# Kernel tuning notes

Measured on AMD Instinct MI355X. Metric: run time of the kernel, lower is better.

The kernel has to match this reference:

```python
import jax, jax.numpy as jnp
import numpy as np

T, B, I, H, O = 512, 128, 512, 1024, 256

def setup_inputs() -> dict:
    key = jax.random.key(0)
    ks = jax.random.split(key, 7)
    s = 1.0 / np.sqrt(H)
    return {
        "seqs": jax.random.normal(ks[0], (T, B, I), dtype=jnp.float32),
        "W_ih": jax.random.uniform(ks[1], (H, I), minval=-s, maxval=s, dtype=jnp.float32),
        "W_hh": jax.random.uniform(ks[2], (H, H), minval=-s, maxval=s, dtype=jnp.float32),
        "b_ih": jax.random.uniform(ks[3], (H,), minval=-s, maxval=s, dtype=jnp.float32),
        "b_hh": jax.random.uniform(ks[4], (H,), minval=-s, maxval=s, dtype=jnp.float32),
        "W_fc": jax.random.uniform(ks[5], (O, H), minval=-s, maxval=s, dtype=jnp.float32),
        "b_fc": jax.random.uniform(ks[6], (O,), minval=-s, maxval=s, dtype=jnp.float32),
    }

def reference(seqs, W_ih, W_hh, b_ih, b_hh, W_fc, b_fc):
    # Precompute input projections for all timesteps in one big GEMM: [T,B,H]
    x_proj = jnp.einsum('tbi,hi->tbh', seqs, W_ih) + b_ih + b_hh

    def step(h, xp):
        h_new = jax.nn.relu(xp + h @ W_hh.T)
        return h_new, None

    h0 = jnp.zeros((seqs.shape[1], W_hh.shape[0]), dtype=seqs.dtype)
    h_final, _ = jax.lax.scan(step, h0, x_proj)
    return h_final @ W_fc.T + b_fc
```

## Files before the change

kernel.cpp:

```cpp
#include <hip/hip_runtime.h>
#include <hip/hip_bf16.h>
#include <stdint.h>

#define T_STEPS 512
#define BATCH   128
#define IN      512
#define HID     1024
#define OUTN    256

typedef __bf16 bf16x8 __attribute__((ext_vector_type(8)));
typedef float  f32x4  __attribute__((ext_vector_type(4)));
typedef unsigned short us8 __attribute__((ext_vector_type(8)));
typedef unsigned int   ui4 __attribute__((ext_vector_type(4)));

__device__ __forceinline__ unsigned short f2bf(float f) {
    uint32_t u = __float_as_uint(f);
    uint32_t r = (u + 0x7fffu + ((u >> 16) & 1u)) >> 16;
    return (unsigned short)r;
}

__device__ __forceinline__ ui4 ld_u128_agent(const void* p) {
    ui4 v;
    asm volatile("global_load_dwordx4 %0, %1, off sc0 sc1"
                 : "=v"(v) : "v"(p) : "memory");
    return v;
}

__device__ __forceinline__ bf16x8 ld_frag(const unsigned short* smem, int row, int kbyte, int rowstride) {
    int off = row * rowstride + (kbyte ^ ((row & 7) << 4));
    return *reinterpret_cast<const bf16x8*>(reinterpret_cast<const char*>(smem) + off);
}

__global__ __launch_bounds__(256, 1) void rnn_persistent(
    const float* __restrict__ seqs, const float* __restrict__ W_ih,
    const float* __restrict__ W_hh, const float* __restrict__ b_ih,
    const float* __restrict__ b_hh, const float* __restrict__ W_fc,
    const float* __restrict__ b_fc, float* __restrict__ out,
    unsigned short* __restrict__ hbuf,
    float* __restrict__ hfinal,
    unsigned int* __restrict__ flags)
{
    const int tid  = threadIdx.x;
    const int lane = tid & 63;
    const int wv   = tid >> 6;
    const int wg   = blockIdx.x;
    const int g    = wg >> 5;
    const int w    = wg & 31;
    const int gr0  = g * 16;
    const int c0   = w * 32;
    const int ln15 = lane & 15;
    const int lk   = lane >> 4;

    __shared__ unsigned short xtile[16 * 512];
    __shared__ float red[4][16][33];
    __shared__ float biasS[32];

    bf16x8 wih[2][4];
    bf16x8 whh[2][8];
    #pragma unroll
    for (int nt = 0; nt < 2; nt++) {
        const int j = c0 + nt * 16 + ln15;
        #pragma unroll
        for (int s = 0; s < 4; s++) {
            const int k = wv * 128 + s * 32 + lk * 8;
            const float* p = W_ih + j * IN + k;
            us8 u;
            #pragma unroll
            for (int e = 0; e < 8; e++) u[e] = f2bf(p[e]);
            wih[nt][s] = __builtin_bit_cast(bf16x8, u);
        }
        #pragma unroll
        for (int s = 0; s < 8; s++) {
            const int k = wv * 256 + s * 32 + lk * 8;
            const float* p = W_hh + j * HID + k;
            us8 u;
            #pragma unroll
            for (int e = 0; e < 8; e++) u[e] = f2bf(p[e]);
            whh[nt][s] = __builtin_bit_cast(bf16x8, u);
        }
    }
    if (tid < 32) biasS[tid] = b_ih[c0 + tid] + b_hh[c0 + tid];

    unsigned int* grp_flags = flags + g * 32 * 16;
    unsigned int* my_flag   = grp_flags + w * 16;

    const int hfrag = ln15 * 2048 + wv * 512 + lk * 16;

    const int xrow[4] = { (tid) >> 6, (tid + 256) >> 6, (tid + 512) >> 6, (tid + 768) >> 6 };
    const int xcol[4] = { (tid) & 63, (tid + 256) & 63, (tid + 512) & 63, (tid + 768) & 63 };

    us8 xbf[4];
    {
        const float* xsrc = seqs + (size_t)gr0 * IN;
        #pragma unroll
        for (int it = 0; it < 4; it++) {
            const float* s4 = xsrc + xrow[it] * IN + xcol[it] * 8;
            float4 a = *reinterpret_cast<const float4*>(s4);
            float4 b = *reinterpret_cast<const float4*>(s4 + 4);
            us8 u;
            u[0]=f2bf(a.x); u[1]=f2bf(a.y); u[2]=f2bf(a.z); u[3]=f2bf(a.w);
            u[4]=f2bf(b.x); u[5]=f2bf(b.y); u[6]=f2bf(b.z); u[7]=f2bf(b.w);
            xbf[it] = u;
        }
    }

    const size_t slotB = (size_t)BATCH * HID * 2;
    char* hbase = reinterpret_cast<char*>(hbuf);

    for (int t = 0; t < T_STEPS; t++) {
        #pragma unroll
        for (int it = 0; it < 4; it++) {
            const int off = xrow[it] * 1024 + ((xcol[it] * 16) ^ ((xrow[it] & 7) << 4));
            *reinterpret_cast<us8*>(reinterpret_cast<char*>(xtile) + off) = xbf[it];
        }

        float4 xr[8];
        {
            const int tn = (t + 1 < T_STEPS) ? t + 1 : t;
            const float* xsrc = seqs + (size_t)tn * (BATCH * IN) + (size_t)gr0 * IN;
            #pragma unroll
            for (int it = 0; it < 4; it++) {
                const float* s4 = xsrc + xrow[it] * IN + xcol[it] * 8;
                xr[2*it]   = *reinterpret_cast<const float4*>(s4);
                xr[2*it+1] = *reinterpret_cast<const float4*>(s4 + 4);
            }
        }

        if (t > 0 && wv == 0 && lane < 32) {
            const unsigned int* f = grp_flags + lane * 16;
            while (__hip_atomic_load(f, __ATOMIC_RELAXED, __HIP_MEMORY_SCOPE_AGENT) < (unsigned)t) {
                __builtin_amdgcn_s_sleep(1);
            }
        }
        __syncthreads();

        ui4 hv[8];
        if (t > 0) {
            const char* hsrc = hbase + (size_t)(t & 1) * slotB + (size_t)gr0 * 2048 + hfrag;
            #pragma unroll
            for (int s = 0; s < 8; s++) hv[s] = ld_u128_agent(hsrc + s * 64);
        }
        __builtin_amdgcn_sched_barrier(0);

        f32x4 acc0 = {0.f, 0.f, 0.f, 0.f};
        f32x4 acc1 = {0.f, 0.f, 0.f, 0.f};
        {
            const int kx0b = wv * 256;
            #pragma unroll
            for (int s = 0; s < 4; s++) {
                bf16x8 a = ld_frag(xtile, ln15, kx0b + s * 64 + lk * 16, 1024);
                acc0 = __builtin_amdgcn_mfma_f32_16x16x32_bf16(a, wih[0][s], acc0, 0, 0, 0);
                acc1 = __builtin_amdgcn_mfma_f32_16x16x32_bf16(a, wih[1][s], acc1, 0, 0, 0);
            }
        }

        if (t > 0) {
            asm volatile("s_waitcnt vmcnt(0)" ::: "memory");
            __builtin_amdgcn_sched_barrier(0);
            #pragma unroll
            for (int s = 0; s < 8; s++) {
                bf16x8 a = __builtin_bit_cast(bf16x8, hv[s]);
                acc0 = __builtin_amdgcn_mfma_f32_16x16x32_bf16(a, whh[0][s], acc0, 0, 0, 0);
                acc1 = __builtin_amdgcn_mfma_f32_16x16x32_bf16(a, whh[1][s], acc1, 0, 0, 0);
            }
        }

        #pragma unroll
        for (int r = 0; r < 4; r++) {
            red[wv][lk * 4 + r][ln15]      = acc0[r];
            red[wv][lk * 4 + r][16 + ln15] = acc1[r];
        }
        __syncthreads();

        const int hrow = tid >> 4;
        const int co2  = (tid & 15) * 2;
        float v0 = red[0][hrow][co2]   + red[1][hrow][co2]   + red[2][hrow][co2]   + red[3][hrow][co2]   + biasS[co2];
        float v1 = red[0][hrow][co2+1] + red[1][hrow][co2+1] + red[2][hrow][co2+1] + red[3][hrow][co2+1] + biasS[co2+1];
        v0 = fmaxf(v0, 0.0f);
        v1 = fmaxf(v1, 0.0f);

        if (t < T_STEPS - 1) {
            unsigned pack = (unsigned)f2bf(v0) | ((unsigned)f2bf(v1) << 16);
            unsigned* dst = reinterpret_cast<unsigned*>(
                hbase + (size_t)((t + 1) & 1) * slotB
                + ((size_t)(gr0 + hrow) * HID + c0 + co2) * 2);
            __hip_atomic_store(dst, pack, __ATOMIC_RELAXED, __HIP_MEMORY_SCOPE_AGENT);
        } else {
            unsigned long long pack = ((unsigned long long)__float_as_uint(v1) << 32) | __float_as_uint(v0);
            unsigned long long* dst = reinterpret_cast<unsigned long long*>(
                hfinal + (size_t)(gr0 + hrow) * HID + c0 + co2);
            __hip_atomic_store(dst, pack, __ATOMIC_RELAXED, __HIP_MEMORY_SCOPE_AGENT);
        }

        asm volatile("s_waitcnt vmcnt(0)" ::: "memory");
        __builtin_amdgcn_sched_barrier(0);
        __syncthreads();
        if (tid == 0) {
            __hip_atomic_store(my_flag, (unsigned)(t + 1), __ATOMIC_RELAXED, __HIP_MEMORY_SCOPE_AGENT);
        }

        #pragma unroll
        for (int it = 0; it < 4; it++) {
            float4 a = xr[2*it], b = xr[2*it+1];
            us8 u;
            u[0]=f2bf(a.x); u[1]=f2bf(a.y); u[2]=f2bf(a.z); u[3]=f2bf(a.w);
            u[4]=f2bf(b.x); u[5]=f2bf(b.y); u[6]=f2bf(b.z); u[7]=f2bf(b.w);
            xbf[it] = u;
        }
    }

    if (wv == 0 && lane < 32) {
        const unsigned int* f = grp_flags + lane * 16;
        while (__hip_atomic_load(f, __ATOMIC_RELAXED, __HIP_MEMORY_SCOPE_AGENT) < (unsigned)T_STEPS) {
            __builtin_amdgcn_s_sleep(1);
        }
    }
    __syncthreads();
    __threadfence();

    {
        const int oi   = tid & 127;
        const int half = tid >> 7;
        const int brow = gr0 + (oi >> 3);
        const int o    = w * 8 + (oi & 7);
        const float* hv2 = hfinal + (size_t)brow * HID + half * 512;
        const float* wf  = W_fc  + (size_t)o * HID + half * 512;
        float sum = 0.f;
        #pragma unroll 4
        for (int k = 0; k < 512; k += 4) {
            float4 hh = *reinterpret_cast<const float4*>(hv2 + k);
            float4 ww = *reinterpret_cast<const float4*>(wf + k);
            sum += hh.x * ww.x + hh.y * ww.y + hh.z * ww.z + hh.w * ww.w;
        }
        float* redf = &red[0][0][0];
        redf[tid] = sum;
        __syncthreads();
        if (tid < 128) {
            out[(size_t)brow * OUTN + o] = redf[tid] + redf[tid + 128] + b_fc[o];
        }
    }
}

extern "C" void kernel_launch(void* const* d_in, const int* in_sizes, int n_in,
                              void* d_out, int out_size, void* d_ws, size_t ws_size,
                              hipStream_t stream) {
    const float* seqs = (const float*)d_in[0];
    const float* W_ih = (const float*)d_in[1];
    const float* W_hh = (const float*)d_in[2];
    const float* b_ih = (const float*)d_in[3];
    const float* b_hh = (const float*)d_in[4];
    const float* W_fc = (const float*)d_in[5];
    const float* b_fc = (const float*)d_in[6];
    float* out = (float*)d_out;

    char* ws = (char*)d_ws;
    unsigned short* hbuf   = (unsigned short*)ws;
    float*          hfinal = (float*)(ws + 524288);
    unsigned int*   flags  = (unsigned int*)(ws + 1048576);

    hipMemsetAsync(flags, 0, 8 * 32 * 64, stream);
    rnn_persistent<<<dim3(256), dim3(256), 0, stream>>>(
        seqs, W_ih, W_hh, b_ih, b_hh, W_fc, b_fc, out, hbuf, hfinal, flags);
}
```

Before: 1.543 ms.

## Add dedicated poller wavefront with per-producer LDS ready flags and streamed h loads

Adds a fifth wavefront that polls the 32 producer flags and publishes per-producer readiness into LDS. Compute wavefronts can then start loading and multiplying each h chunk as soon as its producer finishes, instead of waiting for the whole group behind a block barrier. The h buffer is re-laid out in producer-contiguous 1KB chunks, and the x tile prefetch is moved two steps ahead. The cost is an extra busy-spinning wave, LDS spin loops without sleep, and more complex synchronisation.

```diff
diff --git a/kernel.cpp b/kernel.cpp
--- a/kernel.cpp
+++ b/kernel.cpp
@@ -22,7 +22,13 @@
 __device__ __forceinline__ ui4 ld_u128_agent(const void* p) {
     ui4 v;
     asm volatile("global_load_dwordx4 %0, %1, off sc0 sc1"
-                 : "=v"(v) : "v"(p) : "memory");
+                 : "=&v"(v) : "v"(p) : "memory");
+    return v;
+}
+__device__ __forceinline__ float4 ld_f128(const void* p) {
+    float4 v;
+    asm volatile("global_load_dwordx4 %0, %1, off"
+                 : "=&v"(v) : "v"(p) : "memory");
     return v;
 }
 
@@ -31,7 +37,11 @@
     return *reinterpret_cast<const bf16x8*>(reinterpret_cast<const char*>(smem) + off);
 }
 
-__global__ __launch_bounds__(256, 1) void rnn_persistent(
+__device__ __forceinline__ void lds_wait(const unsigned* p, unsigned t) {
+    while (__hip_atomic_load(p, __ATOMIC_RELAXED, __HIP_MEMORY_SCOPE_WORKGROUP) < t) { }
+}
+
+__global__ __launch_bounds__(320, 1) void rnn_persistent(
     const float* __restrict__ seqs, const float* __restrict__ W_ih,
     const float* __restrict__ W_hh, const float* __restrict__ b_ih,
     const float* __restrict__ b_hh, const float* __restrict__ W_fc,
@@ -54,43 +64,48 @@
     __shared__ unsigned short xtile[16 * 512];
     __shared__ float red[4][16][33];
     __shared__ float biasS[32];
+    __shared__ unsigned ready[32];
 
     bf16x8 wih[2][4];
     bf16x8 whh[2][8];
-    #pragma unroll
-    for (int nt = 0; nt < 2; nt++) {
-        const int j = c0 + nt * 16 + ln15;
+    if (wv < 4) {
         #pragma unroll
-        for (int s = 0; s < 4; s++) {
-            const int k = wv * 128 + s * 32 + lk * 8;
-            const float* p = W_ih + j * IN + k;
-            us8 u;
-            #pragma unroll
-            for (int e = 0; e < 8; e++) u[e] = f2bf(p[e]);
-            wih[nt][s] = __builtin_bit_cast(bf16x8, u);
-        }
-        #pragma unroll
-        for (int s = 0; s < 8; s++) {
-            const int k = wv * 256 + s * 32 + lk * 8;
-            const float* p = W_hh + j * HID + k;
-            us8 u;
-            #pragma unroll
-            for (int e = 0; e < 8; e++) u[e] = f2bf(p[e]);
-            whh[nt][s] = __builtin_bit_cast(bf16x8, u);
-        }
-    }
-    if (tid < 32) biasS[tid] = b_ih[c0 + tid] + b_hh[c0 + tid];
+        for (int nt = 0; nt < 2; nt++) {
+            const int j = c0 + nt * 16 + ln15;
+            #pragma unroll
+            for (int s = 0; s < 4; s++) {
+                const int k = wv * 128 + s * 32 + lk * 8;
+                const float* p = W_ih + j * IN + k;
+                us8 u;
+                #pragma unroll
+                for (int e = 0; e < 8; e++) u[e] = f2bf(p[e]);
+                wih[nt][s] = __builtin_bit_cast(bf16x8, u);
+            }
+            #pragma unroll
+            for (int s = 0; s < 8; s++) {
+                const int k = wv * 256 + s * 32 + lk * 8;
+                const float* p = W_hh + j * HID + k;
+                us8 u;
+                #pragma unroll
+                for (int e = 0; e < 8; e++) u[e] = f2bf(p[e]);
+                whh[nt][s] = __builtin_bit_cast(bf16x8, u);
+            }
+        }
+    }
+    if (tid < 32) {
+        biasS[tid] = b_ih[c0 + tid] + b_hh[c0 + tid];
+        ready[tid] = 0u;
+    }
 
     unsigned int* grp_flags = flags + g * 32 * 16;
     unsigned int* my_flag   = grp_flags + w * 16;
 
-    const int hfrag = ln15 * 2048 + wv * 512 + lk * 16;
-
     const int xrow[4] = { (tid) >> 6, (tid + 256) >> 6, (tid + 512) >> 6, (tid + 768) >> 6 };
     const int xcol[4] = { (tid) & 63, (tid + 256) & 63, (tid + 512) & 63, (tid + 768) & 63 };
 
     us8 xbf[4];
-    {
+    float4 xr[8];
+    if (tid < 256) {
         const float* xsrc = seqs + (size_t)gr0 * IN;
         #pragma unroll
         for (int it = 0; it < 4; it++) {
@@ -102,49 +117,29 @@
             u[4]=f2bf(b.x); u[5]=f2bf(b.y); u[6]=f2bf(b.z); u[7]=f2bf(b.w);
             xbf[it] = u;
         }
-    }
-
-    const size_t slotB = (size_t)BATCH * HID * 2;
-    char* hbase = reinterpret_cast<char*>(hbuf);
-
-    for (int t = 0; t < T_STEPS; t++) {
         #pragma unroll
         for (int it = 0; it < 4; it++) {
             const int off = xrow[it] * 1024 + ((xcol[it] * 16) ^ ((xrow[it] & 7) << 4));
             *reinterpret_cast<us8*>(reinterpret_cast<char*>(xtile) + off) = xbf[it];
         }
-
-        float4 xr[8];
-        {
-            const int tn = (t + 1 < T_STEPS) ? t + 1 : t;
-            const float* xsrc = seqs + (size_t)tn * (BATCH * IN) + (size_t)gr0 * IN;
-            #pragma unroll
-            for (int it = 0; it < 4; it++) {
-                const float* s4 = xsrc + xrow[it] * IN + xcol[it] * 8;
-                xr[2*it]   = *reinterpret_cast<const float4*>(s4);
-                xr[2*it+1] = *reinterpret_cast<const float4*>(s4 + 4);
-            }
-        }
-
-        if (t > 0 && wv == 0 && lane < 32) {
-            const unsigned int* f = grp_flags + lane * 16;
-            while (__hip_atomic_load(f, __ATOMIC_RELAXED, __HIP_MEMORY_SCOPE_AGENT) < (unsigned)t) {
-                __builtin_amdgcn_s_sleep(1);
-            }
-        }
-        __syncthreads();
-
-        ui4 hv[8];
-        if (t > 0) {
-            const char* hsrc = hbase + (size_t)(t & 1) * slotB + (size_t)gr0 * 2048 + hfrag;
-            #pragma unroll
-            for (int s = 0; s < 8; s++) hv[s] = ld_u128_agent(hsrc + s * 64);
-        }
-        __builtin_amdgcn_sched_barrier(0);
-
+        const float* xn = seqs + (size_t)1 * (BATCH * IN) + (size_t)gr0 * IN;
+        #pragma unroll
+        for (int it = 0; it < 4; it++) {
+            const float* s4 = xn + xrow[it] * IN + xcol[it] * 8;
+            xr[2*it]   = ld_f128(s4);
+            xr[2*it+1] = ld_f128(s4 + 4);
+        }
+    }
+    __syncthreads();
+
+    const size_t slotB = 8 * 32 * 1024;
+    char* hbase = reinterpret_cast<char*>(hbuf);
+    const int loff = ln15 * 64 + lk * 16;
+
+    for (int t = 0; t < T_STEPS; t++) {
         f32x4 acc0 = {0.f, 0.f, 0.f, 0.f};
         f32x4 acc1 = {0.f, 0.f, 0.f, 0.f};
-        {
+        if (wv < 4) {
             const int kx0b = wv * 256;
             #pragma unroll
             for (int s = 0; s < 4; s++) {
@@ -154,62 +149,125 @@
             }
         }
 
-        if (t > 0) {
-            asm volatile("s_waitcnt vmcnt(0)" ::: "memory");
-            __builtin_amdgcn_sched_barrier(0);
-            #pragma unroll
-            for (int s = 0; s < 8; s++) {
-                bf16x8 a = __builtin_bit_cast(bf16x8, hv[s]);
-                acc0 = __builtin_amdgcn_mfma_f32_16x16x32_bf16(a, whh[0][s], acc0, 0, 0, 0);
-                acc1 = __builtin_amdgcn_mfma_f32_16x16x32_bf16(a, whh[1][s], acc1, 0, 0, 0);
-            }
-        }
-
-        #pragma unroll
-        for (int r = 0; r < 4; r++) {
-            red[wv][lk * 4 + r][ln15]      = acc0[r];
-            red[wv][lk * 4 + r][16 + ln15] = acc1[r];
-        }
-        __syncthreads();
-
-        const int hrow = tid >> 4;
-        const int co2  = (tid & 15) * 2;
-        float v0 = red[0][hrow][co2]   + red[1][hrow][co2]   + red[2][hrow][co2]   + red[3][hrow][co2]   + biasS[co2];
-        float v1 = red[0][hrow][co2+1] + red[1][hrow][co2+1] + red[2][hrow][co2+1] + red[3][hrow][co2+1] + biasS[co2+1];
-        v0 = fmaxf(v0, 0.0f);
-        v1 = fmaxf(v1, 0.0f);
-
-        if (t < T_STEPS - 1) {
-            unsigned pack = (unsigned)f2bf(v0) | ((unsigned)f2bf(v1) << 16);
-            unsigned* dst = reinterpret_cast<unsigned*>(
-                hbase + (size_t)((t + 1) & 1) * slotB
-                + ((size_t)(gr0 + hrow) * HID + c0 + co2) * 2);
-            __hip_atomic_store(dst, pack, __ATOMIC_RELAXED, __HIP_MEMORY_SCOPE_AGENT);
-        } else {
-            unsigned long long pack = ((unsigned long long)__float_as_uint(v1) << 32) | __float_as_uint(v0);
-            unsigned long long* dst = reinterpret_cast<unsigned long long*>(
-                hfinal + (size_t)(gr0 + hrow) * HID + c0 + co2);
-            __hip_atomic_store(dst, pack, __ATOMIC_RELAXED, __HIP_MEMORY_SCOPE_AGENT);
-        }
-
         asm volatile("s_waitcnt vmcnt(0)" ::: "memory");
         __builtin_amdgcn_sched_barrier(0);
+        if (tid < 256) {
+            #pragma unroll
+            for (int it = 0; it < 4; it++) {
+                float4 a = xr[2*it], b = xr[2*it+1];
+                us8 u;
+                u[0]=f2bf(a.x); u[1]=f2bf(a.y); u[2]=f2bf(a.z); u[3]=f2bf(a.w);
+                u[4]=f2bf(b.x); u[5]=f2bf(b.y); u[6]=f2bf(b.z); u[7]=f2bf(b.w);
+                xbf[it] = u;
+            }
+        }
+
+        if (t > 0) {
+            if (wv == 4) {
+                unsigned long long done = 0;
+                const unsigned int* f = grp_flags + (lane & 31) * 16;
+                for (;;) {
+                    unsigned v = __hip_atomic_load(f, __ATOMIC_RELAXED, __HIP_MEMORY_SCOPE_AGENT);
+                    unsigned long long m  = __ballot(v >= (unsigned)t);
+                    unsigned long long nw = m & ~done;
+                    if (lane < 32 && ((nw >> lane) & 1ull)) {
+                        __hip_atomic_store(&ready[lane], (unsigned)t,
+                                           __ATOMIC_RELAXED, __HIP_MEMORY_SCOPE_WORKGROUP);
+                    }
+                    done = m;
+                    if (m == 0xFFFFFFFFFFFFFFFFull) break;
+                }
+            } else {
+                const char* sb = hbase + (size_t)(t & 1) * slotB + g * 32768
+                               + (wv * 8) * 1024 + loff;
+                lds_wait(&ready[wv * 8], (unsigned)t);
+                ui4 hA = ld_u128_agent(sb);
+                ui4 hB;
+
+#define STAGE(S, CUR, NXT)                                                          \
+                lds_wait(&ready[wv * 8 + (S) + 1], (unsigned)t);                    \
+                NXT = ld_u128_agent(sb + ((S) + 1) * 1024);                         \
+                asm volatile("s_waitcnt vmcnt(1)" ::: "memory");                    \
+                __builtin_amdgcn_sched_barrier(0);                                  \
+                { bf16x8 a_ = __builtin_bit_cast(bf16x8, CUR);                      \
+                  acc0 = __builtin_amdgcn_mfma_f32_16x16x32_bf16(a_, whh[0][S], acc0, 0, 0, 0); \
+                  acc1 = __builtin_amdgcn_mfma_f32_16x16x32_bf16(a_, whh[1][S], acc1, 0, 0, 0); }
+
+                STAGE(0, hA, hB)
+                STAGE(1, hB, hA)
+                STAGE(2, hA, hB)
+                STAGE(3, hB, hA)
+                STAGE(4, hA, hB)
+                STAGE(5, hB, hA)
+                STAGE(6, hA, hB)
+#undef STAGE
+                asm volatile("s_waitcnt vmcnt(0)" ::: "memory");
+                __builtin_amdgcn_sched_barrier(0);
+                {
+                    bf16x8 a_ = __builtin_bit_cast(bf16x8, hB);
+                    acc0 = __builtin_amdgcn_mfma_f32_16x16x32_bf16(a_, whh[0][7], acc0, 0, 0, 0);
+                    acc1 = __builtin_amdgcn_mfma_f32_16x16x32_bf16(a_, whh[1][7], acc1, 0, 0, 0);
+                }
+            }
+        }
+
+        if (wv < 4) {
+            #pragma unroll
+            for (int r = 0; r < 4; r++) {
+                red[wv][lk * 4 + r][ln15]      = acc0[r];
+                red[wv][lk * 4 + r][16 + ln15] = acc1[r];
+            }
+        }
+        __syncthreads();
+
+        if (tid < 256) {
+            const int hrow = tid >> 4;
+            const int co2  = (tid & 15) * 2;
+            float v0 = red[0][hrow][co2]   + red[1][hrow][co2]   + red[2][hrow][co2]   + red[3][hrow][co2]   + biasS[co2];
+            float v1 = red[0][hrow][co2+1] + red[1][hrow][co2+1] + red[2][hrow][co2+1] + red[3][hrow][co2+1] + biasS[co2+1];
+            v0 = fmaxf(v0, 0.0f);
+            v1 = fmaxf(v1, 0.0f);
+            if (t < T_STEPS - 1) {
+                unsigned pack = (unsigned)f2bf(v0) | ((unsigned)f2bf(v1) << 16);
+                unsigned* dst = reinterpret_cast<unsigned*>(
+                    hbase + (size_t)((t + 1) & 1) * slotB + g * 32768 + w * 1024
+                    + hrow * 64 + co2 * 2);
+                __hip_atomic_store(dst, pack, __ATOMIC_RELAXED, __HIP_MEMORY_SCOPE_AGENT);
+            } else {
+                unsigned long long pack = ((unsigned long long)__float_as_uint(v1) << 32) | __float_as_uint(v0);
+                unsigned long long* dst = reinterpret_cast<unsigned long long*>(
+                    hfinal + (size_t)(gr0 + hrow) * HID + c0 + co2);
+                __hip_atomic_store(dst, pack, __ATOMIC_RELAXED, __HIP_MEMORY_SCOPE_AGENT);
+            }
+        }
+
+        asm volatile("s_waitcnt vmcnt(0)" ::: "memory");
+        __builtin_amdgcn_sched_barrier(0);
+        if (tid < 256) {
+            #pragma unroll
+            for (int it = 0; it < 4; it++) {
+                const int off = xrow[it] * 1024 + ((xcol[it] * 16) ^ ((xrow[it] & 7) << 4));
+                *reinterpret_cast<us8*>(reinterpret_cast<char*>(xtile) + off) = xbf[it];
+            }
+        }
         __syncthreads();
         if (tid == 0) {
             __hip_atomic_store(my_flag, (unsigned)(t + 1), __ATOMIC_RELAXED, __HIP_MEMORY_SCOPE_AGENT);
         }
 
-        #pragma unroll
-        for (int it = 0; it < 4; it++) {
-            float4 a = xr[2*it], b = xr[2*it+1];
-            us8 u;
-            u[0]=f2bf(a.x); u[1]=f2bf(a.y); u[2]=f2bf(a.z); u[3]=f2bf(a.w);
-            u[4]=f2bf(b.x); u[5]=f2bf(b.y); u[6]=f2bf(b.z); u[7]=f2bf(b.w);
-            xbf[it] = u;
-        }
-    }
-
-    if (wv == 0 && lane < 32) {
+        if (tid < 256) {
+            const int tn = (t + 2 < T_STEPS) ? t + 2 : T_STEPS - 1;
+            const float* xn = seqs + (size_t)tn * (BATCH * IN) + (size_t)gr0 * IN;
+            #pragma unroll
+            for (int it = 0; it < 4; it++) {
+                const float* s4 = xn + xrow[it] * IN + xcol[it] * 8;
+                xr[2*it]   = ld_f128(s4);
+                xr[2*it+1] = ld_f128(s4 + 4);
+            }
+        }
+    }
+
+    if (wv == 4 && lane < 32) {
         const unsigned int* f = grp_flags + lane * 16;
         while (__hip_atomic_load(f, __ATOMIC_RELAXED, __HIP_MEMORY_SCOPE_AGENT) < (unsigned)T_STEPS) {
             __builtin_amdgcn_s_sleep(1);
@@ -219,23 +277,29 @@
     __threadfence();
 
     {
-        const int oi   = tid & 127;
-        const int half = tid >> 7;
-        const int brow = gr0 + (oi >> 3);
-        const int o    = w * 8 + (oi & 7);
-        const float* hv2 = hfinal + (size_t)brow * HID + half * 512;
-        const float* wf  = W_fc  + (size_t)o * HID + half * 512;
-        float sum = 0.f;
-        #pragma unroll 4
-        for (int k = 0; k < 512; k += 4) {
-            float4 hh = *reinterpret_cast<const float4*>(hv2 + k);
-            float4 ww = *reinterpret_cast<const float4*>(wf + k);
-            sum += hh.x * ww.x + hh.y * ww.y + hh.z * ww.z + hh.w * ww.w;
-        }
-        float* redf = &red[0][0][0];
-        redf[tid] = sum;
+        if (tid < 256) {
+            const int oi   = tid & 127;
+            const int half = tid >> 7;
+            const int brow = gr0 + (oi >> 3);
+            const int o    = w * 8 + (oi & 7);
+            const float* hv2 = hfinal + (size_t)brow * HID + half * 512;
+            const float* wf  = W_fc  + (size_t)o * HID + half * 512;
+            float sum = 0.f;
+            #pragma unroll 4
+            for (int k = 0; k < 512; k += 4) {
+                float4 hh = *reinterpret_cast<const float4*>(hv2 + k);
+                float4 ww = *reinterpret_cast<const float4*>(wf + k);
+                sum += hh.x * ww.x + hh.y * ww.y + hh.z * ww.z + hh.w * ww.w;
+            }
+            float* redf = &red[0][0][0];
+            redf[tid] = sum;
+        }
         __syncthreads();
         if (tid < 128) {
+            const int oi   = tid;
+            const int brow = gr0 + (oi >> 3);
+            const int o    = w * 8 + (oi & 7);
+            float* redf = &red[0][0][0];
             out[(size_t)brow * OUTN + o] = redf[tid] + redf[tid + 128] + b_fc[o];
         }
     }
@@ -259,6 +323,6 @@
     unsigned int*   flags  = (unsigned int*)(ws + 1048576);
 
     hipMemsetAsync(flags, 0, 8 * 32 * 64, stream);
-    rnn_persistent<<<dim3(256), dim3(256), 0, stream>>>(
+    rnn_persistent<<<dim3(256), dim3(320), 0, stream>>>(
         seqs, W_ih, W_hh, b_ih, b_hh, W_fc, b_fc, out, hbuf, hfinal, flags);
 }
```

New measurement: 1.669 ms. 1.08x slower.
